# Performance work log

Hardware: AMD Instinct MI355X
Metric: run time of the kernel (lower is better)

Reference implementation:

```python
import jax, jax.numpy as jnp
import numpy as np

S, B, H, D, G = 2048, 2, 16, 128, 16  # seq, batch, heads, head_dim, v-quant groups


def setup_inputs() -> dict:
    key = jax.random.key(0)
    ks = jax.random.split(key, 9)
    # int8-valued activations stored as float (torch code does .to(torch.int8))
    q = jax.random.randint(ks[0], (S, B, H, D), -128, 128).astype(jnp.float32)
    k = jax.random.randint(ks[1], (S, B, H, D), -128, 128).astype(jnp.float32)
    v = jax.random.randint(ks[2], (S, B, H, D), -128, 128).astype(jnp.float32)
    qmin = jax.random.normal(ks[3], (S, B, H, 1), jnp.float32) * 0.01
    qscale = jax.random.uniform(ks[4], (S, B, H, 1), jnp.float32, 0.005, 0.02)
    kmin = jax.random.normal(ks[5], (S, B, H, 1), jnp.float32) * 0.01
    kscale = jax.random.uniform(ks[6], (S, B, H, 1), jnp.float32, 0.005, 0.02)
    vmin = jax.random.normal(ks[7], (G, B, H, D, 1), jnp.float32) * 0.01
    vscale = jax.random.uniform(ks[8], (G, B, H, D, 1), jnp.float32, 0.005, 0.02)
    return {"query_layer": q, "key_layer": k, "value_layer": v,
            "qmin": qmin, "qscale": qscale, "kmin": kmin, "kscale": kscale,
            "vmin": vmin, "vscale": vscale, "causal": 1}


def _attention(query_layer, key_layer, value_layer, qmin, qscale, kmin, kscale, vmin, vscale, causal):
    # s b h d -> b h s d ; emulate .to(torch.int8) (values are already int8-range ints)
    q = jnp.transpose(query_layer, (1, 2, 0, 3))
    k = jnp.transpose(key_layer, (1, 2, 0, 3))
    v = jnp.transpose(value_layer, (1, 2, 0, 3))
    # per-token quant factors: s b h 1 -> b h s 1
    qm = jnp.transpose(qmin[..., 0], (1, 2, 0))[..., None]
    qs = jnp.transpose(qscale[..., 0], (1, 2, 0))[..., None]
    km = jnp.transpose(kmin[..., 0], (1, 2, 0))[..., None]
    ksc = jnp.transpose(kscale[..., 0], (1, 2, 0))[..., None]
    # attnq_qk: dequantize per-token then QK^T
    qd = q * qs + qm
    kd = k * ksc + km
    scores = jnp.einsum('bhsd,bhtd->bhst', qd, kd)
    # softmaxq: scale by 1/sqrt(128), causal mask, softmax, int8 requant of probs
    scores = scores * jnp.float32(1.0 / np.sqrt(128.0))
    s = scores.shape[-1]
    if causal:
        mask = jnp.tril(jnp.ones((s, s), dtype=bool))
        scores = jnp.where(mask, scores, jnp.float32(-1e9))
    probs = jax.nn.softmax(scores, axis=-1)
    pmin = jnp.min(probs, axis=-1, keepdims=True)
    pmax = jnp.max(probs, axis=-1, keepdims=True)
    pscale = (pmax - pmin) / 255.0 + jnp.float32(1e-12)
    quant_prob = jnp.round((probs - pmin) / pscale)  # int8-range prob codes
    # attnq_pv: dequant probs (per query token) and V (per sequence group) then PV
    pd = quant_prob * pscale + pmin
    vm = jnp.transpose(vmin[..., 0], (1, 2, 0, 3))  # b h g d
    vs = jnp.transpose(vscale[..., 0], (1, 2, 0, 3))
    gs = v.shape[2] // vm.shape[2]  # group size along sequence
    vd = v * jnp.repeat(vs, gs, axis=2) + jnp.repeat(vm, gs, axis=2)
    out = jnp.einsum('bhst,bhtd->bhsd', pd, vd)
    b, h, sq, d = out.shape
    return jnp.transpose(out, (2, 0, 1, 3)).reshape(sq, b, h * d)  # s b (h d)


def reference(query_layer, key_layer, value_layer, qmin, qscale, kmin, kscale, vmin, vscale, causal):
    return _attention(query_layer, key_layer, value_layer, qmin, qscale, kmin, kscale, vmin, vscale, causal)
```

## Files before the change

kernel.cpp:

```cpp
#include <hip/hip_runtime.h>
#include <math.h>


#define S_LEN 2048
#define BATCH 2
#define NH    16
#define HD    128
#define RSTR  4096
#define SCALE2 (0.08838834764831845f * 1.4426950408889634f)
#define EXP2F(x) __builtin_amdgcn_exp2f(x)

typedef int v4i __attribute__((ext_vector_type(4)));
#define MFMA16(a,b,c) __builtin_amdgcn_mfma_i32_16x16x64_i8((a),(b),(c),0,0,0)

#define WS_K8   0u
#define WS_V8T  (8u*1024u*1024u)
#define WS_SQ   (16u*1024u*1024u)
#define WS_SK   (WS_SQ + 256u*1024u)
#define WS_GSV  (WS_SK + 256u*1024u)

__device__ __forceinline__ int sbsum(unsigned p) {
    return (int)(signed char)(p) + (int)(signed char)(p>>8)
         + (int)(signed char)(p>>16) + (int)(signed char)(p>>24);
}

__global__ __launch_bounds__(256) void prep_pack(
    const float* __restrict__ Q, const float* __restrict__ K, const float* __restrict__ V,
    signed char* __restrict__ K8, float* __restrict__ SQs, float* __restrict__ SKs,
    signed char* __restrict__ V8T, float* __restrict__ GSV)
{
    __shared__ int v8i[128*33];
    const int tid = threadIdx.x;
    const int bx  = blockIdx.x;
    if (bx < 16384) {
        const int tensor = bx >> 13;
        const int idx = (bx & 8191)*256 + tid;
        const float* src = tensor ? K : Q;
        int tau = idx >> 5, dg = idx & 31;
        float4 x = *(const float4*)(src + (size_t)tau*128 + 4*dg);
        float ssum = x.x + x.y + x.z + x.w;
        #pragma unroll
        for (int off = 16; off >= 1; off >>= 1) ssum += __shfl_xor(ssum, off);
        if (tensor) {
            int a=(int)x.x, b2=(int)x.y, c=(int)x.z, d=(int)x.w;
            ((int*)K8)[(size_t)tau*32 + dg] = (a&255)|((b2&255)<<8)|((c&255)<<16)|((d&255)<<24);
            if ((tid & 31) == 0) SKs[tau] = ssum;
        } else {
            if ((tid & 31) == 0) SQs[tau] = ssum;
        }
    } else {
        const int bid = bx - 16384;
        const int bh = bid & 31, ck = bid >> 5;
        const int b = bh >> 4, h = bh & 15;
        const int t0 = ck * 128;
        const int boff = b*2048 + h*128;
        #pragma unroll
        for (int it = 0; it < 16; ++it) {
            int idx = tid + it*256;
            int t = idx >> 5, dw = idx & 31;
            float4 x = *(const float4*)(V + (size_t)(t0+t)*RSTR + boff + 4*dw);
            int a=(int)x.x, b2=(int)x.y, c=(int)x.z, d=(int)x.w;
            v8i[t*33 + dw] = (a&255)|((b2&255)<<8)|((c&255)<<16)|((d&255)<<24);
        }
        __syncthreads();
        #pragma unroll
        for (int it = 0; it < 4; ++it) {
            int j = tid + it*256;
            int tg = j & 31, dw = j >> 5;
            unsigned r0 = (unsigned)v8i[(4*tg+0)*33 + dw];
            unsigned r1 = (unsigned)v8i[(4*tg+1)*33 + dw];
            unsigned r2 = (unsigned)v8i[(4*tg+2)*33 + dw];
            unsigned r3 = (unsigned)v8i[(4*tg+3)*33 + dw];
            unsigned x01 = __builtin_amdgcn_perm(r1, r0, 0x05010400u);
            unsigned x23 = __builtin_amdgcn_perm(r3, r2, 0x05010400u);
            unsigned y01 = __builtin_amdgcn_perm(r1, r0, 0x07030602u);
            unsigned y23 = __builtin_amdgcn_perm(r3, r2, 0x07030602u);
            unsigned p[4];
            p[0] = __builtin_amdgcn_perm(x23, x01, 0x05040100u);
            p[1] = __builtin_amdgcn_perm(x23, x01, 0x07060302u);
            p[2] = __builtin_amdgcn_perm(y23, y01, 0x05040100u);
            p[3] = __builtin_amdgcn_perm(y23, y01, 0x07060302u);
            int s[4];
            #pragma unroll
            for (int jj = 0; jj < 4; ++jj) {
                int d = 4*dw + jj;
                *(int*)(V8T + ((size_t)bh*128 + d)*2048 + t0 + 4*tg) = (int)p[jj];
                s[jj] = sbsum(p[jj]);
            }
            #pragma unroll
            for (int off = 1; off < 32; off <<= 1) {
                #pragma unroll
                for (int jj = 0; jj < 4; ++jj) s[jj] += __shfl_xor(s[jj], off);
            }
            if (tg == 0) {
                #pragma unroll
                for (int jj = 0; jj < 4; ++jj)
                    GSV[((size_t)bh*16 + ck)*128 + 4*dw + jj] = (float)s[jj];
            }
        }
    }
}

__global__ __launch_bounds__(256, 2) void attn_main(
    const float* __restrict__ Q,
    const signed char* __restrict__ K8, const signed char* __restrict__ V8T,
    const float* __restrict__ QMN, const float* __restrict__ QSC,
    const float* __restrict__ KMN, const float* __restrict__ KSC,
    const float* __restrict__ VMN, const float* __restrict__ VSC,
    const float* __restrict__ SQs, const float* __restrict__ SKs,
    const float* __restrict__ GSV,
    const int* __restrict__ CAUSAL, float* __restrict__ OUT)
{
    __shared__ __align__(16) signed char q8s[64*144];
    __shared__ __align__(16) signed char k8s[128*144];
    __shared__ __align__(16) signed char v8s[128*144];
    __shared__ __align__(16) signed char pcs[64*144];
    __shared__ float rs_c1[64], rs_c2[64], rs_c3[64];
    __shared__ float rs_mx[64], rs_den[64], rs_mn[64];
    __shared__ float rs_u1[64], rs_w1[64], rs_psc[64], rs_pmn[64];
    __shared__ float ktA[128], ktB[128], ktC[128];
    __shared__ float vsA[128], vsB[128];
    __shared__ float vsumL[128], cgsL[128];

    const int tid  = threadIdx.x;
    const int w    = tid >> 6;
    const int lane = tid & 63;
    const int n    = lane & 15;
    const int quad = lane >> 4;
    const int bhi  = blockIdx.x & 31;
    const int qt   = 31 - (int)(blockIdx.x >> 5);
    const int b    = bhi >> 4, h = bhi & 15;
    const int causal = *CAUSAL;
    const int s0   = qt * 64;
    const int boff = b*2048 + h*128;
    const v4i vzero = {0,0,0,0};
    const v4i ones  = {0x01010101,0x01010101,0x01010101,0x01010101};

    #pragma unroll
    for (int it = 0; it < 8; ++it) {
        int idx = tid + it*256;
        int row = idx >> 5, d4 = (idx & 31) << 2;
        float4 x = *(const float4*)(Q + (size_t)(s0+row)*RSTR + boff + d4);
        int a=(int)x.x, b2=(int)x.y, c=(int)x.z, d=(int)x.w;
        *(int*)(q8s + row*144 + d4) = (a&255)|((b2&255)<<8)|((c&255)<<16)|((d&255)<<24);
    }
    if (tid < 64) {
        int si = (s0 + tid)*32 + bhi;
        float qs = QSC[si], qm = QMN[si];
        rs_c1[tid] = qs; rs_c2[tid] = qm;
        rs_c3[tid] = fmaf(qs, SQs[si], 128.0f*qm);
    }
    __syncthreads();

    const int kt_end = causal ? ((s0 + 63) >> 7) : 15;

    float c1r[4], c2r[4], c3r[4]; int qgr[4];
    #pragma unroll
    for (int r = 0; r < 4; ++r) {
        int qq = 16*w + 4*quad + r;
        c1r[r] = rs_c1[qq]; c2r[r] = rs_c2[qq]; c3r[r] = rs_c3[qq];
        qgr[r] = s0 + qq;
    }
    v4i a0p = *(const v4i*)(q8s + (16*w + n)*144 + 16*quad);
    v4i a1p = *(const v4i*)(q8s + (16*w + n)*144 + 64 + 16*quad);

    float m[4], l[4], mn[4];
    #pragma unroll
    for (int r = 0; r < 4; ++r) { m[r] = -INFINITY; l[r] = 0.f; mn[r] = INFINITY; }

#define P1_TILE(MASKED)                                                          \
  do {                                                                           \
    const int t0g = kt * 128;                                                    \
    __syncthreads();                                                             \
    _Pragma("unroll")                                                            \
    for (int it = 0; it < 4; ++it) {                                             \
        int idx = tid + it*256;                                                  \
        int trow = idx >> 3, doff = (idx & 7) << 4;                              \
        *(uint4*)(k8s + trow*144 + doff) =                                       \
            *(const uint4*)(K8 + ((size_t)(t0g+trow)*32 + bhi)*128 + doff);      \
    }                                                                            \
    if (tid < 128) {                                                             \
        int si = (t0g + tid)*32 + bhi;                                           \
        ktA[tid] = KSC[si]*SCALE2; ktB[tid] = KMN[si]*SCALE2; ktC[tid] = SKs[si];\
    }                                                                            \
    __syncthreads();                                                             \
    float tmax[4], sarr[8][4];                                                   \
    _Pragma("unroll")                                                            \
    for (int r = 0; r < 4; ++r) tmax[r] = -INFINITY;                             \
    _Pragma("unroll")                                                            \
    for (int tb = 0; tb < 8; ++tb) {                                             \
        v4i b0 = *(const v4i*)(k8s + (16*tb + n)*144 + 16*quad);                 \
        v4i b1 = *(const v4i*)(k8s + (16*tb + n)*144 + 64 + 16*quad);            \
        v4i acc = MFMA16(a0p, b0, vzero);                                        \
        acc = MFMA16(a1p, b1, acc);                                              \
        int tl = 16*tb + n;                                                      \
        float kA = ktA[tl], kB = ktB[tl], kC = ktC[tl];                          \
        _Pragma("unroll")                                                        \
        for (int r = 0; r < 4; ++r) {                                            \
            float Sf = (float)acc[r];                                            \
            float sv = fmaf(kA, fmaf(c1r[r], Sf, c2r[r]*kC), kB*c3r[r]);         \
            if (MASKED) sv = (t0g + tl > qgr[r]) ? -INFINITY : sv;               \
            sarr[tb][r] = sv;                                                    \
            tmax[r] = fmaxf(tmax[r], sv);                                        \
            mn[r] = fminf(mn[r], sv);                                            \
        }                                                                        \
    }                                                                            \
    _Pragma("unroll")                                                            \
    for (int r = 0; r < 4; ++r) {                                                \
        float mm = fmaxf(m[r], tmax[r]);                                         \
        if (mm > -INFINITY) {                                                    \
            float e0 = EXP2F(sarr[0][r]-mm) + EXP2F(sarr[1][r]-mm);              \
            float e1 = EXP2F(sarr[2][r]-mm) + EXP2F(sarr[3][r]-mm);              \
            float e2 = EXP2F(sarr[4][r]-mm) + EXP2F(sarr[5][r]-mm);              \
            float e3 = EXP2F(sarr[6][r]-mm) + EXP2F(sarr[7][r]-mm);              \
            l[r] = fmaf(l[r], EXP2F(m[r]-mm), (e0+e1)+(e2+e3));                  \
            m[r] = mm;                                                           \
        }                                                                        \
    }                                                                            \
  } while (0)

    {
        int kt;
        for (kt = 0; kt < kt_end; ++kt) P1_TILE(false);
        kt = kt_end;
        if (causal) P1_TILE(true); else P1_TILE(false);
    }

    #pragma unroll
    for (int r = 0; r < 4; ++r) {
        #pragma unroll
        for (int off = 1; off < 16; off <<= 1) {
            float m2 = __shfl_xor(m[r], off);
            float l2 = __shfl_xor(l[r], off);
            float n2 = __shfl_xor(mn[r], off);
            float mm = fmaxf(m[r], m2);
            if (mm > -INFINITY) l[r] = l[r]*EXP2F(m[r]-mm) + l2*EXP2F(m2-mm);
            m[r] = mm;
            mn[r] = fminf(mn[r], n2);
        }
        if (n == 0) {
            int qq = 16*w + 4*quad + r;
            rs_mx[qq] = m[r]; rs_den[qq] = l[r]; rs_mn[qq] = mn[r];
        }
    }
    __syncthreads();
    if (tid < 64) {
        float mx = rs_mx[tid], den = rs_den[tid], mnv = rs_mn[tid];
        float invd = 1.0f/den;
        int s = s0 + tid;
        bool hasmask = (causal != 0) && (s < S_LEN-1);
        float pmin = hasmask ? 0.0f : EXP2F(mnv - mx)*invd;
        float psc  = (invd - pmin)/255.0f + 1e-12f;
        float ipsc = 1.0f/psc;
        rs_u1[tid] = invd*ipsc; rs_w1[tid] = -pmin*ipsc;
        rs_psc[tid] = psc; rs_pmn[tid] = pmin;
    } else if (tid >= 128) {
        int d = tid - 128;
        float vsum = 0.f, cgs = 0.f;
        #pragma unroll
        for (int g = 0; g < 16; ++g) {
            float gs = GSV[((size_t)bhi*16 + g)*128 + d];
            int vi = ((g*BATCH + b)*NH + h)*HD + d;
            float vs = VSC[vi], vm = VMN[vi];
            vsum = fmaf(vs, gs, fmaf(128.0f, vm, vsum));
            if (g <= kt_end) cgs = fmaf(128.0f*vs, gs, fmaf(16384.0f, vm, cgs));
        }
        vsumL[d] = vsum; cgsL[d] = cgs;
    }
    __syncthreads();

    v4i qb0[4], qb1[4];
    float qc1[4], qc2[4], qc3[4], qmxn[4], qu1[4], qw1[4];
    int qgq[4];
    #pragma unroll
    for (int cb = 0; cb < 4; ++cb) {
        int qcol = 16*cb + n;
        qb0[cb] = *(const v4i*)(q8s + qcol*144 + 16*quad);
        qb1[cb] = *(const v4i*)(q8s + qcol*144 + 64 + 16*quad);
        qc1[cb] = rs_c1[qcol]; qc2[cb] = rs_c2[qcol]; qc3[cb] = rs_c3[qcol];
        qmxn[cb] = -rs_mx[qcol]; qu1[cb] = rs_u1[qcol]; qw1[cb] = rs_w1[qcol];
        qgq[cb] = s0 + qcol;
    }

    float outa[4][8];
    #pragma unroll
    for (int r = 0; r < 4; ++r)
        #pragma unroll
        for (int db = 0; db < 8; ++db) outa[r][db] = 0.f;

#define P2_TILE(MASKED)                                                          \
  do {                                                                           \
    const int t0g = kt * 128;                                                    \
    __syncthreads();                      \
    _Pragma("unroll")                                                            \
    for (int it = 0; it < 4; ++it) {                                             \
        int idx = tid + it*256;                                                  \
        int trow = idx >> 3, doff = (idx & 7) << 4;                              \
        *(uint4*)(v8s + trow*144 + doff) =                                       \
            *(const uint4*)(V8T + ((size_t)bhi*128 + trow)*2048 + t0g + doff);   \
    }                                                                            \
    if (tid < 128) {                                                             \
        int si = (t0g + tid)*32 + bhi;                                           \
        ktA[tid] = KSC[si]*SCALE2; ktB[tid] = KMN[si]*SCALE2; ktC[tid] = SKs[si];\
    } else {                                                                     \
        int d = tid - 128;                                                       \
        int vi = ((kt*BATCH + b)*NH + h)*HD + d;                                 \
        vsA[d] = VSC[vi]; vsB[d] = VMN[vi];                                      \
    }                                                                            \
    __syncthreads();                                                             \
    _Pragma("unroll")                                                            \
    for (int rb = 0; rb < 2; ++rb) {                                             \
        int trow = 32*w + 16*rb;                                                 \
        const signed char* kp = K8 + ((size_t)(t0g+trow+n)*32 + bhi)*128         \
                                   + 16*quad;                                    \
        v4i a0 = *(const v4i*)kp;              \
        v4i a1 = *(const v4i*)(kp + 64);                                         \
        float ksr[4], kmr[4], skr[4];                                            \
        int tgb = t0g + trow + 4*quad;                                           \
        _Pragma("unroll")                                                        \
        for (int r = 0; r < 4; ++r) {                                            \
            int tl = trow + 4*quad + r;                                          \
            ksr[r] = ktA[tl]; kmr[r] = ktB[tl]; skr[r] = ktC[tl];                \
        }                                                                        \
        _Pragma("unroll")                                                        \
        for (int cb = 0; cb < 4; ++cb) {                                         \
            v4i acc = MFMA16(a0, qb0[cb], vzero);                                \
            acc = MFMA16(a1, qb1[cb], acc);                                      \
            int cby[4];                                                          \
            _Pragma("unroll")                                                    \
            for (int r = 0; r < 4; ++r) {                                        \
                float Sf = (float)acc[r];                                        \
                float x = fmaf(ksr[r], fmaf(qc1[cb], Sf, qc2[cb]*skr[r]),        \
                               fmaf(kmr[r], qc3[cb], qmxn[cb]));                 \
                if (MASKED) x = (tgb + r > qgq[cb]) ? -INFINITY : x;             \
                float e = EXP2F(x);                                              \
                float f = fmaf(e, qu1[cb], qw1[cb]) + 8388608.0f;   \
                cby[r] = __float_as_int(f);                                      \
            }                                                                    \
            unsigned t01 = __builtin_amdgcn_perm((unsigned)cby[1],               \
                                                 (unsigned)cby[0], 0x00000400u); \
            unsigned t23 = __builtin_amdgcn_perm((unsigned)cby[3],               \
                                                 (unsigned)cby[2], 0x04000000u); \
            int packed = (int)(__builtin_amdgcn_perm(t23, t01, 0x07060100u)      \
                               ^ 0x80808080u);          \
            *(int*)(pcs + (16*cb + n)*144 + trow + 4*quad) = packed;             \
        }                                                                        \
    }                                                                            \
    __syncthreads();                                                             \
    {                                                                            \
        v4i a0 = *(const v4i*)(pcs + (16*w + n)*144 + 16*quad);                  \
        v4i a1 = *(const v4i*)(pcs + (16*w + n)*144 + 64 + 16*quad);             \
        v4i c1a = MFMA16(a0, ones, vzero);                                       \
        c1a = MFMA16(a1, ones, c1a);                                             \
        float c1f[4];                                                            \
        _Pragma("unroll")                                                        \
        for (int r = 0; r < 4; ++r) c1f[r] = (float)c1a[r];                      \
        _Pragma("unroll")                                                        \
        for (int db = 0; db < 8; ++db) {                                         \
            v4i b0 = *(const v4i*)(v8s + (16*db + n)*144 + 16*quad);             \
            v4i b1 = *(const v4i*)(v8s + (16*db + n)*144 + 64 + 16*quad);        \
            v4i cv = MFMA16(a0, b0, vzero);                                      \
            cv = MFMA16(a1, b1, cv);                                             \
            int d = 16*db + n;                                                   \
            float vs = vsA[d], vm = vsB[d];                                      \
            _Pragma("unroll")                                                    \
            for (int r = 0; r < 4; ++r)                                          \
                outa[r][db] = fmaf(vs, (float)cv[r],                             \
                                   fmaf(vm, c1f[r], outa[r][db]));               \
        }                                                                        \
    }                                                                            \
  } while (0)

    {
        int kt;
        for (kt = 0; kt < kt_end; ++kt) P2_TILE(false);
        kt = kt_end;
        if (causal) P2_TILE(true); else P2_TILE(false);
    }

    float pscr[4], pmnr[4];
    #pragma unroll
    for (int r = 0; r < 4; ++r) {
        int qq = 16*w + 4*quad + r;
        pscr[r] = rs_psc[qq]; pmnr[r] = rs_pmn[qq];
    }
    #pragma unroll
    for (int db = 0; db < 8; ++db) {
        int d = 16*db + n;
        float vsum = vsumL[d];
        float cgs  = cgsL[d];
        #pragma unroll
        for (int r = 0; r < 4; ++r) {
            int s = s0 + 16*w + 4*quad + r;
            OUT[(size_t)s*RSTR + boff + d] = fmaf(pscr[r], outa[r][db] + cgs, pmnr[r]*vsum);
        }
    }
}

extern "C" void kernel_launch(void* const* d_in, const int* in_sizes, int n_in,
                              void* d_out, int out_size, void* d_ws, size_t ws_size,
                              hipStream_t stream) {
    (void)in_sizes; (void)n_in; (void)out_size; (void)ws_size;
    const float* Q   = (const float*)d_in[0];
    const float* K   = (const float*)d_in[1];
    const float* V   = (const float*)d_in[2];
    const float* QMN = (const float*)d_in[3];
    const float* QSC = (const float*)d_in[4];
    const float* KMN = (const float*)d_in[5];
    const float* KSC = (const float*)d_in[6];
    const float* VMN = (const float*)d_in[7];
    const float* VSC = (const float*)d_in[8];
    const int*   CS  = (const int*)d_in[9];
    float* out = (float*)d_out;

    char* ws = (char*)d_ws;
    signed char* K8  = (signed char*)(ws + WS_K8);
    signed char* V8T = (signed char*)(ws + WS_V8T);
    float* SQs  = (float*)(ws + WS_SQ);
    float* SKs  = (float*)(ws + WS_SK);
    float* GSVp = (float*)(ws + WS_GSV);

    prep_pack<<<16384 + 512, 256, 0, stream>>>(Q, K, V, K8, SQs, SKs, V8T, GSVp);
    attn_main<<<1024, 256, 0, stream>>>(Q, K8, V8T, QMN, QSC, KMN, KSC, VMN, VSC,
                                        SQs, SKs, GSVp, CS, out);
}
```

Measured before the change: 252.8 us.

## Read K directly from global, double-buffer K scales, and restructure the prep grid

The attention kernel no longer stages K tiles in LDS. The first pass reads int8 K fragments straight from global memory, and the per-key scale, min and sum vectors are double-buffered so the next tile's values are prefetched while the current tile is processed. This removes a pair of block barriers per tile in both passes, frees LDS, and raises the launch-bounds occupancy hint from 2 to 3. The prep kernel now launches the V-transpose blocks first and has each Q/K block handle 8 chunks, so it launches far fewer blocks. The costs are more global/L2 traffic for repeated K fragment loads and added risk around the barrier removed after the V tile is staged.

After: 347.3 us. 1.37x slower.

```diff
diff --git a/kernel.cpp b/kernel.cpp
--- a/kernel.cpp
+++ b/kernel.cpp
@@ -32,24 +32,28 @@
     __shared__ int v8i[128*33];
     const int tid = threadIdx.x;
     const int bx  = blockIdx.x;
-    if (bx < 16384) {
-        const int tensor = bx >> 13;
-        const int idx = (bx & 8191)*256 + tid;
-        const float* src = tensor ? K : Q;
-        int tau = idx >> 5, dg = idx & 31;
-        float4 x = *(const float4*)(src + (size_t)tau*128 + 4*dg);
-        float ssum = x.x + x.y + x.z + x.w;
-        #pragma unroll
-        for (int off = 16; off >= 1; off >>= 1) ssum += __shfl_xor(ssum, off);
-        if (tensor) {
-            int a=(int)x.x, b2=(int)x.y, c=(int)x.z, d=(int)x.w;
-            ((int*)K8)[(size_t)tau*32 + dg] = (a&255)|((b2&255)<<8)|((c&255)<<16)|((d&255)<<24);
-            if ((tid & 31) == 0) SKs[tau] = ssum;
-        } else {
-            if ((tid & 31) == 0) SQs[tau] = ssum;
+    if (bx >= 512) {
+        const int base = (bx - 512)*256 + tid;
+        #pragma unroll
+        for (int rep = 0; rep < 8; ++rep) {
+            const int tensor = rep >> 2;
+            const int idx = base + (rep & 3)*524288;
+            const float* src = tensor ? K : Q;
+            int tau = idx >> 5, dg = idx & 31;
+            float4 x = *(const float4*)(src + (size_t)tau*128 + 4*dg);
+            float ssum = x.x + x.y + x.z + x.w;
+            #pragma unroll
+            for (int off = 16; off >= 1; off >>= 1) ssum += __shfl_xor(ssum, off);
+            if (tensor) {
+                int a=(int)x.x, b2=(int)x.y, c=(int)x.z, d=(int)x.w;
+                ((int*)K8)[(size_t)tau*32 + dg] = (a&255)|((b2&255)<<8)|((c&255)<<16)|((d&255)<<24);
+                if ((tid & 31) == 0) SKs[tau] = ssum;
+            } else {
+                if ((tid & 31) == 0) SQs[tau] = ssum;
+            }
         }
     } else {
-        const int bid = bx - 16384;
+        const int bid = bx;
         const int bh = bid & 31, ck = bid >> 5;
         const int b = bh >> 4, h = bh & 15;
         const int t0 = ck * 128;
@@ -101,7 +105,7 @@
     }
 }
 
-__global__ __launch_bounds__(256, 2) void attn_main(
+__global__ __launch_bounds__(256, 3) void attn_main(
     const float* __restrict__ Q,
     const signed char* __restrict__ K8, const signed char* __restrict__ V8T,
     const float* __restrict__ QMN, const float* __restrict__ QSC,
@@ -112,13 +116,12 @@
     const int* __restrict__ CAUSAL, float* __restrict__ OUT)
 {
     __shared__ __align__(16) signed char q8s[64*144];
-    __shared__ __align__(16) signed char k8s[128*144];
     __shared__ __align__(16) signed char v8s[128*144];
     __shared__ __align__(16) signed char pcs[64*144];
     __shared__ float rs_c1[64], rs_c2[64], rs_c3[64];
     __shared__ float rs_mx[64], rs_den[64], rs_mn[64];
     __shared__ float rs_u1[64], rs_w1[64], rs_psc[64], rs_pmn[64];
-    __shared__ float ktA[128], ktB[128], ktC[128];
+    __shared__ float ktA[2][128], ktB[2][128], ktC[2][128];
     __shared__ float vsA[128], vsB[128];
     __shared__ float vsumL[128], cgsL[128];
 
@@ -149,6 +152,10 @@
         float qs = QSC[si], qm = QMN[si];
         rs_c1[tid] = qs; rs_c2[tid] = qm;
         rs_c3[tid] = fmaf(qs, SQs[si], 128.0f*qm);
+    } else if (tid >= 128) {
+        int d = tid - 128;
+        int si = d*32 + bhi;
+        ktA[0][d] = KSC[si]*SCALE2; ktB[0][d] = KMN[si]*SCALE2; ktC[0][d] = SKs[si];
     }
     __syncthreads();
 
@@ -171,30 +178,26 @@
 #define P1_TILE(MASKED)                                                          \
   do {                                                                           \
     const int t0g = kt * 128;                                                    \
-    __syncthreads();                                                             \
-    _Pragma("unroll")                                                            \
-    for (int it = 0; it < 4; ++it) {                                             \
-        int idx = tid + it*256;                                                  \
-        int trow = idx >> 3, doff = (idx & 7) << 4;                              \
-        *(uint4*)(k8s + trow*144 + doff) =                                       \
-            *(const uint4*)(K8 + ((size_t)(t0g+trow)*32 + bhi)*128 + doff);      \
-    }                                                                            \
-    if (tid < 128) {                                                             \
-        int si = (t0g + tid)*32 + bhi;                                           \
-        ktA[tid] = KSC[si]*SCALE2; ktB[tid] = KMN[si]*SCALE2; ktC[tid] = SKs[si];\
-    }                                                                            \
-    __syncthreads();                                                             \
+    const int cur = kt & 1;                                                      \
+    if (kt < kt_end && tid < 128) {                                              \
+        int si = (t0g + 128 + tid)*32 + bhi;                                     \
+        ktA[cur^1][tid] = KSC[si]*SCALE2;                                        \
+        ktB[cur^1][tid] = KMN[si]*SCALE2;                                        \
+        ktC[cur^1][tid] = SKs[si];                                               \
+    }                                                                            \
     float tmax[4], sarr[8][4];                                                   \
     _Pragma("unroll")                                                            \
     for (int r = 0; r < 4; ++r) tmax[r] = -INFINITY;                             \
     _Pragma("unroll")                                                            \
     for (int tb = 0; tb < 8; ++tb) {                                             \
-        v4i b0 = *(const v4i*)(k8s + (16*tb + n)*144 + 16*quad);                 \
-        v4i b1 = *(const v4i*)(k8s + (16*tb + n)*144 + 64 + 16*quad);            \
+        const signed char* kp = K8 + ((size_t)(t0g + 16*tb + n)*32 + bhi)*128    \
+                                   + 16*quad;                                    \
+        v4i b0 = *(const v4i*)kp;                                                \
+        v4i b1 = *(const v4i*)(kp + 64);                                         \
         v4i acc = MFMA16(a0p, b0, vzero);                                        \
         acc = MFMA16(a1p, b1, acc);                                              \
         int tl = 16*tb + n;                                                      \
-        float kA = ktA[tl], kB = ktB[tl], kC = ktC[tl];                          \
+        float kA = ktA[cur][tl], kB = ktB[cur][tl], kC = ktC[cur][tl];           \
         _Pragma("unroll")                                                        \
         for (int r = 0; r < 4; ++r) {                                            \
             float Sf = (float)acc[r];                                            \
@@ -217,6 +220,7 @@
             m[r] = mm;                                                           \
         }                                                                        \
     }                                                                            \
+    __syncthreads();                                                             \
   } while (0)
 
     {
@@ -266,6 +270,8 @@
             if (g <= kt_end) cgs = fmaf(128.0f*vs, gs, fmaf(16384.0f, vm, cgs));
         }
         vsumL[d] = vsum; cgsL[d] = cgs;
+        int si = d*32 + bhi;
+        ktA[0][d] = KSC[si]*SCALE2; ktB[0][d] = KMN[si]*SCALE2; ktC[0][d] = SKs[si];
     }
     __syncthreads();
 
@@ -291,7 +297,8 @@
 #define P2_TILE(MASKED)                                                          \
   do {                                                                           \
     const int t0g = kt * 128;                                                    \
-    __syncthreads();                      \
+    const int cur = kt & 1;                                                      \
+    __syncthreads();                  \
     _Pragma("unroll")                                                            \
     for (int it = 0; it < 4; ++it) {                                             \
         int idx = tid + it*256;                                                  \
@@ -300,14 +307,17 @@
             *(const uint4*)(V8T + ((size_t)bhi*128 + trow)*2048 + t0g + doff);   \
     }                                                                            \
     if (tid < 128) {                                                             \
-        int si = (t0g + tid)*32 + bhi;                                           \
-        ktA[tid] = KSC[si]*SCALE2; ktB[tid] = KMN[si]*SCALE2; ktC[tid] = SKs[si];\
+        if (kt < kt_end) {                                                       \
+            int si = (t0g + 128 + tid)*32 + bhi;                                 \
+            ktA[cur^1][tid] = KSC[si]*SCALE2;                                    \
+            ktB[cur^1][tid] = KMN[si]*SCALE2;                                    \
+            ktC[cur^1][tid] = SKs[si];                                           \
+        }                                                                        \
     } else {                                                                     \
         int d = tid - 128;                                                       \
         int vi = ((kt*BATCH + b)*NH + h)*HD + d;                                 \
         vsA[d] = VSC[vi]; vsB[d] = VMN[vi];                                      \
     }                                                                            \
-    __syncthreads();                                                             \
     _Pragma("unroll")                                                            \
     for (int rb = 0; rb < 2; ++rb) {                                             \
         int trow = 32*w + 16*rb;                                                 \
@@ -320,7 +330,7 @@
         _Pragma("unroll")                                                        \
         for (int r = 0; r < 4; ++r) {                                            \
             int tl = trow + 4*quad + r;                                          \
-            ksr[r] = ktA[tl]; kmr[r] = ktB[tl]; skr[r] = ktC[tl];                \
+            ksr[r] = ktA[cur][tl]; kmr[r] = ktB[cur][tl]; skr[r] = ktC[cur][tl]; \
         }                                                                        \
         _Pragma("unroll")                                                        \
         for (int cb = 0; cb < 4; ++cb) {                                         \
@@ -420,7 +430,7 @@
     float* SKs  = (float*)(ws + WS_SK);
     float* GSVp = (float*)(ws + WS_GSV);
 
-    prep_pack<<<16384 + 512, 256, 0, stream>>>(Q, K, V, K8, SQs, SKs, V8T, GSVp);
+    prep_pack<<<512 + 2048, 256, 0, stream>>>(Q, K, V, K8, SQs, SKs, V8T, GSVp);
     attn_main<<<1024, 256, 0, stream>>>(Q, K8, V8T, QMN, QSC, KMN, KSC, VMN, VSC,
                                         SQs, SKs, GSVp, CS, out);
 }
```

## Compute per-row Q sums via MFMA in attention kernel, drop Q prep pass

Applied to the files above, without the earlier changes.

The pre-pass no longer reads the whole Q tensor just to compute per-token Q row sums. Those sums are now computed inside the attention kernel with two int8 MFMAs against a ones vector, using the Q tile already packed in shared memory. The prep kernel is also split into separate V-transpose and K-pack launches, and the K kernel has each thread handle 8 float4s instead of 1. This removes one full-tensor read of Q (about 16 MB) at the cost of an extra launch and an extra block barrier in the main kernel.

Result: faster. 243.3 us (-3.8%).

```diff
diff --git a/kernel.cpp b/kernel.cpp
--- a/kernel.cpp
+++ b/kernel.cpp
@@ -15,8 +15,7 @@
 
 #define WS_K8   0u
 #define WS_V8T  (8u*1024u*1024u)
-#define WS_SQ   (16u*1024u*1024u)
-#define WS_SK   (WS_SQ + 256u*1024u)
+#define WS_SK   (16u*1024u*1024u)
 #define WS_GSV  (WS_SK + 256u*1024u)
 
 __device__ __forceinline__ int sbsum(unsigned p) {
@@ -24,79 +23,77 @@
          + (int)(signed char)(p>>16) + (int)(signed char)(p>>24);
 }
 
-__global__ __launch_bounds__(256) void prep_pack(
-    const float* __restrict__ Q, const float* __restrict__ K, const float* __restrict__ V,
-    signed char* __restrict__ K8, float* __restrict__ SQs, float* __restrict__ SKs,
-    signed char* __restrict__ V8T, float* __restrict__ GSV)
+__global__ __launch_bounds__(256) void prep_k(const float* __restrict__ K,
+                                              signed char* __restrict__ K8,
+                                              float* __restrict__ SKs)
+{
+    const int base = blockIdx.x*2048 + threadIdx.x;
+    #pragma unroll
+    for (int rep = 0; rep < 8; ++rep) {
+        int idx = base + rep*256;
+        float4 x = *(const float4*)(K + (size_t)idx*4);
+        int a=(int)x.x, b=(int)x.y, c=(int)x.z, d=(int)x.w;
+        ((int*)K8)[idx] = (a&255)|((b&255)<<8)|((c&255)<<16)|((d&255)<<24);
+        float s = x.x + x.y + x.z + x.w;
+        #pragma unroll
+        for (int off = 16; off >= 1; off >>= 1) s += __shfl_xor(s, off);
+        if ((threadIdx.x & 31) == 0) SKs[idx >> 5] = s;
+    }
+}
+
+__global__ __launch_bounds__(256) void prep_v(const float* __restrict__ V,
+                                              signed char* __restrict__ V8T,
+                                              float* __restrict__ GSV)
 {
     __shared__ int v8i[128*33];
     const int tid = threadIdx.x;
-    const int bx  = blockIdx.x;
-    if (bx < 16384) {
-        const int tensor = bx >> 13;
-        const int idx = (bx & 8191)*256 + tid;
-        const float* src = tensor ? K : Q;
-        int tau = idx >> 5, dg = idx & 31;
-        float4 x = *(const float4*)(src + (size_t)tau*128 + 4*dg);
-        float ssum = x.x + x.y + x.z + x.w;
-        #pragma unroll
-        for (int off = 16; off >= 1; off >>= 1) ssum += __shfl_xor(ssum, off);
-        if (tensor) {
-            int a=(int)x.x, b2=(int)x.y, c=(int)x.z, d=(int)x.w;
-            ((int*)K8)[(size_t)tau*32 + dg] = (a&255)|((b2&255)<<8)|((c&255)<<16)|((d&255)<<24);
-            if ((tid & 31) == 0) SKs[tau] = ssum;
-        } else {
-            if ((tid & 31) == 0) SQs[tau] = ssum;
-        }
-    } else {
-        const int bid = bx - 16384;
-        const int bh = bid & 31, ck = bid >> 5;
-        const int b = bh >> 4, h = bh & 15;
-        const int t0 = ck * 128;
-        const int boff = b*2048 + h*128;
-        #pragma unroll
-        for (int it = 0; it < 16; ++it) {
-            int idx = tid + it*256;
-            int t = idx >> 5, dw = idx & 31;
-            float4 x = *(const float4*)(V + (size_t)(t0+t)*RSTR + boff + 4*dw);
-            int a=(int)x.x, b2=(int)x.y, c=(int)x.z, d=(int)x.w;
-            v8i[t*33 + dw] = (a&255)|((b2&255)<<8)|((c&255)<<16)|((d&255)<<24);
-        }
-        __syncthreads();
-        #pragma unroll
-        for (int it = 0; it < 4; ++it) {
-            int j = tid + it*256;
-            int tg = j & 31, dw = j >> 5;
-            unsigned r0 = (unsigned)v8i[(4*tg+0)*33 + dw];
-            unsigned r1 = (unsigned)v8i[(4*tg+1)*33 + dw];
-            unsigned r2 = (unsigned)v8i[(4*tg+2)*33 + dw];
-            unsigned r3 = (unsigned)v8i[(4*tg+3)*33 + dw];
-            unsigned x01 = __builtin_amdgcn_perm(r1, r0, 0x05010400u);
-            unsigned x23 = __builtin_amdgcn_perm(r3, r2, 0x05010400u);
-            unsigned y01 = __builtin_amdgcn_perm(r1, r0, 0x07030602u);
-            unsigned y23 = __builtin_amdgcn_perm(r3, r2, 0x07030602u);
-            unsigned p[4];
-            p[0] = __builtin_amdgcn_perm(x23, x01, 0x05040100u);
-            p[1] = __builtin_amdgcn_perm(x23, x01, 0x07060302u);
-            p[2] = __builtin_amdgcn_perm(y23, y01, 0x05040100u);
-            p[3] = __builtin_amdgcn_perm(y23, y01, 0x07060302u);
-            int s[4];
+    const int bid = blockIdx.x;
+    const int bh = bid & 31, ck = bid >> 5;
+    const int b = bh >> 4, h = bh & 15;
+    const int t0 = ck * 128;
+    const int boff = b*2048 + h*128;
+    #pragma unroll
+    for (int it = 0; it < 16; ++it) {
+        int idx = tid + it*256;
+        int t = idx >> 5, dw = idx & 31;
+        float4 x = *(const float4*)(V + (size_t)(t0+t)*RSTR + boff + 4*dw);
+        int a=(int)x.x, b2=(int)x.y, c=(int)x.z, d=(int)x.w;
+        v8i[t*33 + dw] = (a&255)|((b2&255)<<8)|((c&255)<<16)|((d&255)<<24);
+    }
+    __syncthreads();
+    #pragma unroll
+    for (int it = 0; it < 4; ++it) {
+        int j = tid + it*256;
+        int tg = j & 31, dw = j >> 5;
+        unsigned r0 = (unsigned)v8i[(4*tg+0)*33 + dw];
+        unsigned r1 = (unsigned)v8i[(4*tg+1)*33 + dw];
+        unsigned r2 = (unsigned)v8i[(4*tg+2)*33 + dw];
+        unsigned r3 = (unsigned)v8i[(4*tg+3)*33 + dw];
+        unsigned x01 = __builtin_amdgcn_perm(r1, r0, 0x05010400u);
+        unsigned x23 = __builtin_amdgcn_perm(r3, r2, 0x05010400u);
+        unsigned y01 = __builtin_amdgcn_perm(r1, r0, 0x07030602u);
+        unsigned y23 = __builtin_amdgcn_perm(r3, r2, 0x07030602u);
+        unsigned p[4];
+        p[0] = __builtin_amdgcn_perm(x23, x01, 0x05040100u);
+        p[1] = __builtin_amdgcn_perm(x23, x01, 0x07060302u);
+        p[2] = __builtin_amdgcn_perm(y23, y01, 0x05040100u);
+        p[3] = __builtin_amdgcn_perm(y23, y01, 0x07060302u);
+        int s[4];
+        #pragma unroll
+        for (int jj = 0; jj < 4; ++jj) {
+            int d = 4*dw + jj;
+            *(int*)(V8T + ((size_t)bh*128 + d)*2048 + t0 + 4*tg) = (int)p[jj];
+            s[jj] = sbsum(p[jj]);
+        }
+        #pragma unroll
+        for (int off = 1; off < 32; off <<= 1) {
             #pragma unroll
-            for (int jj = 0; jj < 4; ++jj) {
-                int d = 4*dw + jj;
-                *(int*)(V8T + ((size_t)bh*128 + d)*2048 + t0 + 4*tg) = (int)p[jj];
-                s[jj] = sbsum(p[jj]);
-            }
+            for (int jj = 0; jj < 4; ++jj) s[jj] += __shfl_xor(s[jj], off);
+        }
+        if (tg == 0) {
             #pragma unroll
-            for (int off = 1; off < 32; off <<= 1) {
-                #pragma unroll
-                for (int jj = 0; jj < 4; ++jj) s[jj] += __shfl_xor(s[jj], off);
-            }
-            if (tg == 0) {
-                #pragma unroll
-                for (int jj = 0; jj < 4; ++jj)
-                    GSV[((size_t)bh*16 + ck)*128 + 4*dw + jj] = (float)s[jj];
-            }
+            for (int jj = 0; jj < 4; ++jj)
+                GSV[((size_t)bh*16 + ck)*128 + 4*dw + jj] = (float)s[jj];
         }
     }
 }
@@ -107,8 +104,7 @@
     const float* __restrict__ QMN, const float* __restrict__ QSC,
     const float* __restrict__ KMN, const float* __restrict__ KSC,
     const float* __restrict__ VMN, const float* __restrict__ VSC,
-    const float* __restrict__ SQs, const float* __restrict__ SKs,
-    const float* __restrict__ GSV,
+    const float* __restrict__ SKs, const float* __restrict__ GSV,
     const int* __restrict__ CAUSAL, float* __restrict__ OUT)
 {
     __shared__ __align__(16) signed char q8s[64*144];
@@ -146,13 +142,27 @@
     }
     if (tid < 64) {
         int si = (s0 + tid)*32 + bhi;
-        float qs = QSC[si], qm = QMN[si];
-        rs_c1[tid] = qs; rs_c2[tid] = qm;
-        rs_c3[tid] = fmaf(qs, SQs[si], 128.0f*qm);
+        rs_c1[tid] = QSC[si]; rs_c2[tid] = QMN[si];
     }
     __syncthreads();
 
     const int kt_end = causal ? ((s0 + 63) >> 7) : 15;
+
+    v4i a0p = *(const v4i*)(q8s + (16*w + n)*144 + 16*quad);
+    v4i a1p = *(const v4i*)(q8s + (16*w + n)*144 + 64 + 16*quad);
+
+    {
+        v4i qsum = MFMA16(a0p, ones, vzero);
+        qsum = MFMA16(a1p, ones, qsum);
+        if (n == 0) {
+            #pragma unroll
+            for (int r = 0; r < 4; ++r) {
+                int qq = 16*w + 4*quad + r;
+                rs_c3[qq] = fmaf(rs_c1[qq], (float)qsum[r], 128.0f*rs_c2[qq]);
+            }
+        }
+    }
+    __syncthreads();
 
     float c1r[4], c2r[4], c3r[4]; int qgr[4];
     #pragma unroll
@@ -161,8 +171,6 @@
         c1r[r] = rs_c1[qq]; c2r[r] = rs_c2[qq]; c3r[r] = rs_c3[qq];
         qgr[r] = s0 + qq;
     }
-    v4i a0p = *(const v4i*)(q8s + (16*w + n)*144 + 16*quad);
-    v4i a1p = *(const v4i*)(q8s + (16*w + n)*144 + 64 + 16*quad);
 
     float m[4], l[4], mn[4];
     #pragma unroll
@@ -416,11 +424,11 @@
     char* ws = (char*)d_ws;
     signed char* K8  = (signed char*)(ws + WS_K8);
     signed char* V8T = (signed char*)(ws + WS_V8T);
-    float* SQs  = (float*)(ws + WS_SQ);
     float* SKs  = (float*)(ws + WS_SK);
     float* GSVp = (float*)(ws + WS_GSV);
 
-    prep_pack<<<16384 + 512, 256, 0, stream>>>(Q, K, V, K8, SQs, SKs, V8T, GSVp);
+    prep_v<<<512, 256, 0, stream>>>(V, V8T, GSVp);
+    prep_k<<<1024, 256, 0, stream>>>(K, K8, SKs);
     attn_main<<<1024, 256, 0, stream>>>(Q, K8, V8T, QMN, QSC, KMN, KSC, VMN, VSC,
-                                        SQs, SKs, GSVp, CS, out);
+                                        SKs, GSVp, CS, out);
 }
```
